# Kernel optimization log

Measured on AMD Instinct MI355X. Metric: run time of the kernel, lower is better.

## Reference

```python
import jax, jax.numpy as jnp
import numpy as np

B, D, X, K = 256, 128, 1_000_000, 100


def setup_inputs() -> dict:
    key = jax.random.key(0)
    k1, k2 = jax.random.split(key)
    query_embeddings = jax.random.normal(k1, (B, D), dtype=jnp.float32)
    item_embeddings_t = jax.random.normal(k2, (D, X), dtype=jnp.float32)
    item_ids = jnp.arange(X, dtype=jnp.int64).reshape(1, X)
    return {
        "query_embeddings": query_embeddings,
        "item_embeddings_t": item_embeddings_t,
        "item_ids": item_ids,
        "k": K,
    }


def reference(query_embeddings, item_embeddings_t, item_ids, k):
    # [B, X] inner-product scores
    all_logits = jnp.matmul(query_embeddings, item_embeddings_t)
    # top-k along the corpus axis (lax.top_k returns sorted descending)
    topk_logits, topk_indices = jax.lax.top_k(all_logits, k)
    topk_item_ids = item_ids[0][topk_indices]  # [B, k]
    return topk_logits, topk_item_ids
```

## Files before the change

kernel.cpp:

```cpp
#include <hip/hip_runtime.h>
#include <hip/hip_bf16.h>
#include <math.h>

#define XT      1000000
#define DQ      128
#define BQ      256
#define TI      64
#define NTILES  15625
#define TPB     16
#define NBLK    977
#define CHUNK   16
#define NCH     62500
#define NCHP    62528
#define CAP     256
#define NCAND   (CAP * CHUNK)
#define KTOP    100
#define DELTA   0.3f
#define ZLO     3.0f
#define BINS    512
#define BINW    0.005f
#define K4BINS  1024
#define K4SEL   512

typedef float f32x4 __attribute__((ext_vector_type(4)));
typedef short bf16x8 __attribute__((ext_vector_type(8)));

__device__ __forceinline__ unsigned ordf(float f) {
  unsigned u = __float_as_uint(f);
  return (u & 0x80000000u) ? ~u : (u ^ 0x80000000u);
}
__device__ __forceinline__ float unordf(unsigned k) {
  unsigned bits = (k & 0x80000000u) ? (k ^ 0x80000000u) : ~k;
  return __uint_as_float(bits);
}
__device__ __forceinline__ unsigned long long packkv(float v, unsigned id) {
  return ((unsigned long long)ordf(v) << 32) | (unsigned long long)(~id);
}
__device__ __forceinline__ float pk_val(unsigned long long e) { return unordf((unsigned)(e >> 32)); }
__device__ __forceinline__ unsigned pk_id(unsigned long long e) { return ~(unsigned)(e & 0xFFFFFFFFu); }

__device__ __forceinline__ unsigned short f2bf(float f) {
  unsigned u = __float_as_uint(f);
  u += 0x7FFFu + ((u >> 16) & 1u);
  return (unsigned short)(u >> 16);
}
__device__ __forceinline__ unsigned cvt_pk_bf16(float a, float b) {
  unsigned r;
  asm("v_cvt_pk_bf16_f32 %0, %1, %2" : "=v"(r) : "v"(a), "v"(b));
  return r;
}
__device__ __forceinline__ float bf_to_f(unsigned us) {
  return __uint_as_float(us << 16);
}

template <int N>
__device__ void bitonic_sort(unsigned long long* buf) {
  for (int k = 2; k <= N; k <<= 1) {
    for (int j = k >> 1; j > 0; j >>= 1) {
      for (int e = threadIdx.x; e < N; e += blockDim.x) {
        int p = e ^ j;
        if (p > e) {
          unsigned long long a = buf[e], b = buf[p];
          bool up = ((e & k) == 0);
          if (up ? (a > b) : (a < b)) { buf[e] = b; buf[p] = a; }
        }
      }
      __syncthreads();
    }
  }
}

__global__ void p0_qprep(const float* __restrict__ Q, unsigned short* __restrict__ Qp,
                         float* __restrict__ norms, uint4* __restrict__ ghist4) {
  const int q = blockIdx.x, d = threadIdx.x;
  ghist4[q * DQ + d] = make_uint4(0, 0, 0, 0);
  float v = Q[q * DQ + d];
  Qp[q * DQ + d] = f2bf(v);
  float ss = v * v;
#pragma unroll
  for (int m = 1; m < 64; m <<= 1) ss += __shfl_xor(ss, m);
  __shared__ float part[2];
  if ((d & 63) == 0) part[d >> 6] = ss;
  __syncthreads();
  if (d == 0) norms[q] = sqrtf(part[0] + part[1]);
}

__device__ __forceinline__ unsigned xs_off(int x, int d) {
  unsigned byte = (unsigned)(x * 256 + d * 2);
  unsigned slot = (unsigned)((((x >> 2) & 3) << 1) | (x & 1));
  return byte ^ (slot << 4);
}

__global__ __launch_bounds__(256, 2) void k1_filter(
    const unsigned short* __restrict__ Qp, const float* __restrict__ It,
    const float* __restrict__ norms, unsigned short* __restrict__ M,
    int* __restrict__ ghist) {
  __shared__ __align__(16) unsigned Xs32[2][4096];
  __shared__ __align__(16) unsigned short Ms[32][256];
  const int t = threadIdx.x;
  const int xg = (t & 15) * 4;
  const int dbase = (t >> 4) * 8;
  const int l = t & 63, w = t >> 6;
  const int wq = w * 64;
  const int lm = l & 15, h = l >> 4;
  const int tile0 = blockIdx.x * TPB;

  bf16x8 qfr[4][4];
#pragma unroll
  for (int n = 0; n < 4; ++n)
#pragma unroll
    for (int b = 0; b < 4; ++b)
      qfr[n][b] = *(const bf16x8*)&Qp[(size_t)(wq + b * 16 + lm) * DQ + n * 32 + h * 8];
  float invq[4];
#pragma unroll
  for (int b = 0; b < 4; ++b) invq[b] = 1.0f / norms[wq + b * 16 + lm];

  float4 st[8];
  {
    int x0 = tile0 * TI;
    bool ok = (x0 < XT);
#pragma unroll
    for (int r = 0; r < 8; ++r)
      st[r] = ok ? *(const float4*)&It[(size_t)(dbase + r) * XT + x0 + xg]
                 : make_float4(0.f, 0.f, 0.f, 0.f);
  }

  for (int tt = 0; tt < TPB; ++tt) {
    unsigned* xsb = &Xs32[tt & 1][0];
#pragma unroll
    for (int j = 0; j < 4; ++j) {
      unsigned wv0 = cvt_pk_bf16(((const float*)&st[0])[j], ((const float*)&st[1])[j]);
      unsigned wv1 = cvt_pk_bf16(((const float*)&st[2])[j], ((const float*)&st[3])[j]);
      unsigned wv2 = cvt_pk_bf16(((const float*)&st[4])[j], ((const float*)&st[5])[j]);
      unsigned wv3 = cvt_pk_bf16(((const float*)&st[6])[j], ((const float*)&st[7])[j]);
      *(uint4*)((char*)xsb + xs_off(xg + j, dbase)) = make_uint4(wv0, wv1, wv2, wv3);
    }
    if (tt + 1 < TPB) {
      int x0 = (tile0 + tt + 1) * TI;
      bool ok = (x0 < XT);
#pragma unroll
      for (int r = 0; r < 8; ++r)
        st[r] = ok ? *(const float4*)&It[(size_t)(dbase + r) * XT + x0 + xg]
                   : make_float4(0.f, 0.f, 0.f, 0.f);
    }
    __syncthreads();

    f32x4 acc[4][4];
#pragma unroll
    for (int a = 0; a < 4; ++a)
#pragma unroll
      for (int b = 0; b < 4; ++b) acc[a][b] = (f32x4){0.f, 0.f, 0.f, 0.f};

#pragma unroll
    for (int n = 0; n < 4; ++n) {
      bf16x8 afr[4];
#pragma unroll
      for (int a = 0; a < 4; ++a)
        afr[a] = *(const bf16x8*)((const char*)xsb + xs_off(a * 16 + lm, n * 32 + h * 8));
#pragma unroll
      for (int b = 0; b < 4; ++b)
#pragma unroll
        for (int a = 0; a < 4; ++a)
          acc[a][b] = __builtin_amdgcn_mfma_f32_16x16x32_bf16(afr[a], qfr[n][b], acc[a][b], 0, 0, 0);
    }

#pragma unroll
    for (int a = 0; a < 4; ++a)
#pragma unroll
      for (int b = 0; b < 4; ++b) {
        f32x4 v = acc[a][b];
        float m0 = fmaxf(fmaxf(v.x, v.y), fmaxf(v.z, v.w));
        m0 = fmaxf(m0, __shfl_xor(m0, 16));
        m0 = fmaxf(m0, __shfl_xor(m0, 32));
        if (l < 16) {
          Ms[(tt & 7) * 4 + a][wq + b * 16 + lm] =
              (unsigned short)(cvt_pk_bf16(m0, 0.f) & 0xffffu);
          float z = m0 * invq[b];
          if (z >= ZLO) {
            int bin = (int)((z - ZLO) * (1.0f / BINW));
            if (bin > BINS - 1) bin = BINS - 1;
            atomicAdd(&ghist[(wq + b * 16 + lm) * BINS + bin], 1);
          }
        }
      }

    if ((tt & 7) == 7) {
      __syncthreads();
      const uint4* srcv = (const uint4*)&Ms[0][0];
      uint4* dstv = (uint4*)(M + ((size_t)tile0 * 4 + (size_t)(tt >> 3) * 32) * 256);
#pragma unroll
      for (int i = 0; i < 4; ++i) dstv[t + i * 256] = srcv[t + i * 256];
    }
  }
}

__global__ __launch_bounds__(512) void k2b_thr(
    const int* __restrict__ ghist, const float* __restrict__ norms,
    float* __restrict__ thrArr, int* __restrict__ cnt) {
  const int q = blockIdx.x, b = threadIdx.x;
  __shared__ int sfx[BINS];
  sfx[b] = ghist[q * BINS + b];
  __syncthreads();
  for (int off = 1; off < BINS; off <<= 1) {
    int v = (b + off < BINS) ? sfx[b + off] : 0;
    __syncthreads();
    sfx[b] += v;
    __syncthreads();
  }
  bool p = sfx[b] >= KTOP;
  bool pn = (b < BINS - 1) ? (sfx[b + 1] >= KTOP) : false;
  if (b == 0) {
    cnt[q] = 0;
    if (sfx[0] < KTOP) thrArr[q] = -3.0e38f;
  }
  if (p && !pn)
    thrArr[q] = (ZLO + (float)(b - 1) * BINW) * norms[q] - DELTA;
}

__global__ __launch_bounds__(256) void k2c_emit(
    const unsigned short* __restrict__ M, const float* __restrict__ thrArr,
    int* __restrict__ list, int* __restrict__ cnt) {
  const int t = threadIdx.x;
  __shared__ float s_thr[BQ];
  s_thr[t] = thrArr[t];
  __syncthreads();
  const int c0 = blockIdx.x * 64;
  const uint4* src = (const uint4*)(M + (size_t)c0 * 256);
  for (int i = t; i < 2048; i += 256) {
    uint4 v = src[i];
    const int q0 = (i & 31) * 8;
    const int c = c0 + (i >> 5);
    unsigned uu[4] = {v.x, v.y, v.z, v.w};
#pragma unroll
    for (int m = 0; m < 4; ++m) {
#pragma unroll
      for (int s = 0; s < 2; ++s) {
        float val = bf_to_f(s ? (uu[m] >> 16) : (uu[m] & 0xffffu));
        int q = q0 + m * 2 + s;
        if (val >= s_thr[q]) {
          int pos = atomicAdd(&cnt[q], 1);
          if (pos < CAP) list[q * CAP + pos] = c;
        }
      }
    }
  }
}

__global__ __launch_bounds__(256) void k3_rescore(
    const float* __restrict__ Q, const float* __restrict__ It,
    const int* __restrict__ list, const int* __restrict__ cnt_in,
    unsigned long long* __restrict__ cand) {
  const int q = blockIdx.x >> 2;
  const int sub = blockIdx.x & 3;
  __shared__ float qv[DQ];
  if (threadIdx.x < DQ) qv[threadIdx.x] = Q[q * DQ + threadIdx.x];
  __syncthreads();
  const int s = threadIdx.x >> 2;
  const int j = threadIdx.x & 3;
  const int gs = sub * 64 + s;
  int n = cnt_in[q];
  if (n > CAP) n = CAP;
  unsigned long long o0 = 0ULL, o1 = 0ULL, o2 = 0ULL, o3 = 0ULL;
  if (gs < n) {
    const int chunk = list[q * CAP + gs];
    const int xb = chunk * CHUNK + j * 4;
    float a0 = 0.f, a1 = 0.f, a2 = 0.f, a3 = 0.f;
#pragma unroll 8
    for (int d = 0; d < DQ; ++d) {
      float4 v = *(const float4*)&It[(size_t)d * XT + xb];
      float qd = qv[d];
      a0 = fmaf(qd, v.x, a0);
      a1 = fmaf(qd, v.y, a1);
      a2 = fmaf(qd, v.z, a2);
      a3 = fmaf(qd, v.w, a3);
    }
    o0 = packkv(a0, (unsigned)(xb + 0));
    o1 = packkv(a1, (unsigned)(xb + 1));
    o2 = packkv(a2, (unsigned)(xb + 2));
    o3 = packkv(a3, (unsigned)(xb + 3));
  }
  unsigned long long* dst = &cand[(size_t)q * NCAND + gs * CHUNK + j * 4];
  dst[0] = o0; dst[1] = o1; dst[2] = o2; dst[3] = o3;
}

__global__ __launch_bounds__(1024) void k4_final(
    const unsigned long long* __restrict__ cand, const float* __restrict__ thrArr,
    float* __restrict__ out) {
  const int q = blockIdx.x;
  const int t = threadIdx.x;
  __shared__ int hist[K4BINS];
  __shared__ unsigned long long sel[K4SEL];
  __shared__ int scnt, bstar;
  hist[t] = 0;
  if (t < K4SEL) sel[t] = 0ULL;
  if (t == 0) { scnt = 0; bstar = 0; }
  const float base = thrArr[q];
  unsigned long long e[4];
  float vv[4];
#pragma unroll
  for (int i = 0; i < 4; ++i) {
    e[i] = cand[(size_t)q * NCAND + t + i * 1024];
    vv[i] = pk_val(e[i]);
  }
  __syncthreads();
#pragma unroll
  for (int i = 0; i < 4; ++i) {
    float d = (vv[i] - base) * 256.0f;
    int b = (d >= 1.0f) ? ((d < (float)(K4BINS - 1)) ? (int)d : (K4BINS - 1)) : 0;
    if (b > 0) atomicAdd(&hist[b], 1);
  }
  __syncthreads();
  for (int off = 1; off < K4BINS; off <<= 1) {
    int v = (t + off < K4BINS) ? hist[t + off] : 0;
    __syncthreads();
    hist[t] += v;
    __syncthreads();
  }
  {
    bool p = hist[t] >= KTOP;
    bool pn = (t < K4BINS - 1) ? (hist[t + 1] >= KTOP) : false;
    if (p && !pn) bstar = t;
  }
  __syncthreads();
  const int bs = bstar;
#pragma unroll
  for (int i = 0; i < 4; ++i) {
    float d = (vv[i] - base) * 256.0f;
    int b = (d >= 1.0f) ? ((d < (float)(K4BINS - 1)) ? (int)d : (K4BINS - 1)) : 0;
    if (b >= bs && e[i] != 0ULL) {
      int pos = atomicAdd(&scnt, 1);
      if (pos < K4SEL) sel[pos] = e[i];
    }
  }
  __syncthreads();
  bitonic_sort<K4SEL>(sel);
  for (int r = t; r < KTOP; r += 1024) {
    unsigned long long ee = sel[K4SEL - 1 - r];
    out[q * KTOP + r] = pk_val(ee);
    out[BQ * KTOP + q * KTOP + r] = (float)pk_id(ee);
  }
}

extern "C" void kernel_launch(void* const* d_in, const int* in_sizes, int n_in,
                              void* d_out, int out_size, void* d_ws, size_t ws_size,
                              hipStream_t stream) {
  const float* Q = (const float*)d_in[0];
  const float* It = (const float*)d_in[1];
  float* out = (float*)d_out;
  char* ws = (char*)d_ws;
  unsigned short* M = (unsigned short*)ws;
  int* ghist = (int*)(ws + 32014336);
  float* thrArr = (float*)(ws + 32538624);
  int* list = (int*)(ws + 32539648);
  int* cnt = (int*)(ws + 32801792);
  float* norms = (float*)(ws + 32802816);
  unsigned short* Qp = (unsigned short*)(ws + 32803840);
  unsigned long long* cand = (unsigned long long*)(ws + 33554432);

  p0_qprep<<<dim3(BQ), dim3(DQ), 0, stream>>>(Q, Qp, norms, (uint4*)ghist);
  k1_filter<<<dim3(NBLK), dim3(256), 0, stream>>>(Qp, It, norms, M, ghist);
  k2b_thr<<<dim3(BQ), dim3(512), 0, stream>>>(ghist, norms, thrArr, cnt);
  k2c_emit<<<dim3(NBLK), dim3(256), 0, stream>>>(M, thrArr, list, cnt);
  k3_rescore<<<dim3(BQ * 4), dim3(256), 0, stream>>>(Q, It, list, cnt, cand);
  k4_final<<<dim3(BQ), dim3(1024), 0, stream>>>(cand, thrArr, out);
}
```

Measured before the change: 295.4 us.

## Fuse rescore and final top-k kernels, keeping candidates in shared memory

```diff
diff --git a/kernel.cpp b/kernel.cpp
--- a/kernel.cpp
+++ b/kernel.cpp
@@ -19,7 +19,7 @@
 #define ZLO     3.0f
 #define BINS    512
 #define BINW    0.005f
-#define K4BINS  1024
+#define K4BINS  512
 #define K4SEL   512
 
 typedef float f32x4 __attribute__((ext_vector_type(4)));
@@ -246,23 +246,29 @@
   }
 }
 
-__global__ __launch_bounds__(256) void k3_rescore(
+__global__ __launch_bounds__(512) void k34_fused(
     const float* __restrict__ Q, const float* __restrict__ It,
     const int* __restrict__ list, const int* __restrict__ cnt_in,
-    unsigned long long* __restrict__ cand) {
-  const int q = blockIdx.x >> 2;
-  const int sub = blockIdx.x & 3;
+    const float* __restrict__ thrArr, float* __restrict__ out) {
+  const int q = blockIdx.x;
+  const int t = threadIdx.x;
   __shared__ float qv[DQ];
-  if (threadIdx.x < DQ) qv[threadIdx.x] = Q[q * DQ + threadIdx.x];
-  __syncthreads();
-  const int s = threadIdx.x >> 2;
-  const int j = threadIdx.x & 3;
-  const int gs = sub * 64 + s;
+  __shared__ unsigned long long cb[NCAND];
+  __shared__ int hist[K4BINS];
+  __shared__ unsigned long long sel[K4SEL];
+  __shared__ int scnt, bstar;
+  if (t < DQ) qv[t] = Q[q * DQ + t];
+  for (int i = t; i < K4BINS; i += 512) hist[i] = 0;
+  for (int i = t; i < K4SEL; i += 512) sel[i] = 0ULL;
+  if (t == 0) { scnt = 0; bstar = 0; }
   int n = cnt_in[q];
   if (n > CAP) n = CAP;
-  unsigned long long o0 = 0ULL, o1 = 0ULL, o2 = 0ULL, o3 = 0ULL;
-  if (gs < n) {
-    const int chunk = list[q * CAP + gs];
+  const int nc = n * CHUNK;
+  __syncthreads();
+
+  for (int task = t; task < n * 4; task += 512) {
+    const int chunk = list[q * CAP + (task >> 2)];
+    const int j = task & 3;
     const int xb = chunk * CHUNK + j * 4;
     float a0 = 0.f, a1 = 0.f, a2 = 0.f, a3 = 0.f;
 #pragma unroll 8
@@ -274,38 +280,18 @@
       a2 = fmaf(qd, v.z, a2);
       a3 = fmaf(qd, v.w, a3);
     }
-    o0 = packkv(a0, (unsigned)(xb + 0));
-    o1 = packkv(a1, (unsigned)(xb + 1));
-    o2 = packkv(a2, (unsigned)(xb + 2));
-    o3 = packkv(a3, (unsigned)(xb + 3));
-  }
-  unsigned long long* dst = &cand[(size_t)q * NCAND + gs * CHUNK + j * 4];
-  dst[0] = o0; dst[1] = o1; dst[2] = o2; dst[3] = o3;
-}
-
-__global__ __launch_bounds__(1024) void k4_final(
-    const unsigned long long* __restrict__ cand, const float* __restrict__ thrArr,
-    float* __restrict__ out) {
-  const int q = blockIdx.x;
-  const int t = threadIdx.x;
-  __shared__ int hist[K4BINS];
-  __shared__ unsigned long long sel[K4SEL];
-  __shared__ int scnt, bstar;
-  hist[t] = 0;
-  if (t < K4SEL) sel[t] = 0ULL;
-  if (t == 0) { scnt = 0; bstar = 0; }
+    unsigned long long* dst = &cb[(task >> 2) * CHUNK + j * 4];
+    dst[0] = packkv(a0, (unsigned)(xb + 0));
+    dst[1] = packkv(a1, (unsigned)(xb + 1));
+    dst[2] = packkv(a2, (unsigned)(xb + 2));
+    dst[3] = packkv(a3, (unsigned)(xb + 3));
+  }
+  __syncthreads();
+
   const float base = thrArr[q];
-  unsigned long long e[4];
-  float vv[4];
-#pragma unroll
-  for (int i = 0; i < 4; ++i) {
-    e[i] = cand[(size_t)q * NCAND + t + i * 1024];
-    vv[i] = pk_val(e[i]);
-  }
-  __syncthreads();
-#pragma unroll
-  for (int i = 0; i < 4; ++i) {
-    float d = (vv[i] - base) * 256.0f;
+  for (int i = t; i < nc; i += 512) {
+    float v = pk_val(cb[i]);
+    float d = (v - base) * 128.0f;
     int b = (d >= 1.0f) ? ((d < (float)(K4BINS - 1)) ? (int)d : (K4BINS - 1)) : 0;
     if (b > 0) atomicAdd(&hist[b], 1);
   }
@@ -323,21 +309,22 @@
   }
   __syncthreads();
   const int bs = bstar;
-#pragma unroll
-  for (int i = 0; i < 4; ++i) {
-    float d = (vv[i] - base) * 256.0f;
+  for (int i = t; i < nc; i += 512) {
+    unsigned long long e = cb[i];
+    float v = pk_val(e);
+    float d = (v - base) * 128.0f;
     int b = (d >= 1.0f) ? ((d < (float)(K4BINS - 1)) ? (int)d : (K4BINS - 1)) : 0;
-    if (b >= bs && e[i] != 0ULL) {
+    if (b >= bs && e != 0ULL) {
       int pos = atomicAdd(&scnt, 1);
-      if (pos < K4SEL) sel[pos] = e[i];
+      if (pos < K4SEL) sel[pos] = e;
     }
   }
   __syncthreads();
   bitonic_sort<K4SEL>(sel);
-  for (int r = t; r < KTOP; r += 1024) {
-    unsigned long long ee = sel[K4SEL - 1 - r];
-    out[q * KTOP + r] = pk_val(ee);
-    out[BQ * KTOP + q * KTOP + r] = (float)pk_id(ee);
+  if (t < KTOP) {
+    unsigned long long ee = sel[K4SEL - 1 - t];
+    out[q * KTOP + t] = pk_val(ee);
+    out[BQ * KTOP + q * KTOP + t] = (float)pk_id(ee);
   }
 }
 
@@ -355,12 +342,10 @@
   int* cnt = (int*)(ws + 32801792);
   float* norms = (float*)(ws + 32802816);
   unsigned short* Qp = (unsigned short*)(ws + 32803840);
-  unsigned long long* cand = (unsigned long long*)(ws + 33554432);
 
   p0_qprep<<<dim3(BQ), dim3(DQ), 0, stream>>>(Q, Qp, norms, (uint4*)ghist);
   k1_filter<<<dim3(NBLK), dim3(256), 0, stream>>>(Qp, It, norms, M, ghist);
   k2b_thr<<<dim3(BQ), dim3(512), 0, stream>>>(ghist, norms, thrArr, cnt);
   k2c_emit<<<dim3(NBLK), dim3(256), 0, stream>>>(M, thrArr, list, cnt);
-  k3_rescore<<<dim3(BQ * 4), dim3(256), 0, stream>>>(Q, It, list, cnt, cand);
-  k4_final<<<dim3(BQ), dim3(1024), 0, stream>>>(cand, thrArr, out);
-}
+  k34_fused<<<dim3(BQ), dim3(512), 0, stream>>>(Q, It, list, cnt, thrArr, out);
+}
```

Measured after the change: 261.3 us. 1.13x faster.
